# Kernel optimization log

Hardware: AMD Instinct MI355X
Metric: run time of the kernel (lower is better)

Reference implementation:

```python
import jax, jax.numpy as jnp
import numpy as np

NUM_USERS = 100000
NUM_MOVIES = 20000
FEAT = 256
H = 64
E = 2000000
EL = 500000


def _seg_mean(msg, dst, n):
    # scatter-mean aggregation: sum per destination node / neighbor count (clamped to 1)
    s = jax.ops.segment_sum(msg, dst, num_segments=n)
    c = jax.ops.segment_sum(jnp.ones((dst.shape[0], 1), msg.dtype), dst, num_segments=n)
    return s / jnp.maximum(c, 1.0)


def _sage(x_src, x_dst, src, dst, wl, bl, wr):
    # PyG SAGEConv (mean aggr): lin_l(mean_j x_j) + lin_r(x_i)
    mean = _seg_mean(x_src[src], dst, x_dst.shape[0])  # [N_dst, H]
    return mean @ wl + bl + x_dst @ wr


def _l2norm(x):
    n = jnp.linalg.norm(x, axis=-1, keepdims=True)
    return x / jnp.maximum(n, 1e-12)


def setup_inputs() -> dict:
    key = jax.random.key(0)
    ks = jax.random.split(key, 24)
    s = 0.02
    d = {
        'movie_x': jax.random.normal(ks[0], (NUM_MOVIES, FEAT), jnp.float32),
        'user_emb': jax.random.normal(ks[1], (NUM_USERS, H), jnp.float32) * s,
        'proj_w': jax.random.normal(ks[2], (FEAT, H), jnp.float32) * s,
        'proj_b': jnp.zeros((H,), jnp.float32),
        'c1_um_wl': jax.random.normal(ks[3], (H, H), jnp.float32) * s,
        'c1_um_bl': jnp.zeros((H,), jnp.float32),
        'c1_um_wr': jax.random.normal(ks[4], (H, H), jnp.float32) * s,
        'c1_mu_wl': jax.random.normal(ks[5], (H, H), jnp.float32) * s,
        'c1_mu_bl': jnp.zeros((H,), jnp.float32),
        'c1_mu_wr': jax.random.normal(ks[6], (H, H), jnp.float32) * s,
        'c2_um_wl': jax.random.normal(ks[7], (H, H), jnp.float32) * s,
        'c2_um_bl': jnp.zeros((H,), jnp.float32),
        'c2_um_wr': jax.random.normal(ks[8], (H, H), jnp.float32) * s,
        'c2_mu_wl': jax.random.normal(ks[9], (H, H), jnp.float32) * s,
        'c2_mu_bl': jnp.zeros((H,), jnp.float32),
        'c2_mu_wr': jax.random.normal(ks[10], (H, H), jnp.float32) * s,
        'dec_w1': jax.random.normal(ks[11], (2 * H, H), jnp.float32) * s,
        'dec_b1': jnp.zeros((H,), jnp.float32),
        'dec_w2': jax.random.normal(ks[12], (H, 1), jnp.float32) * s,
        'dec_b2': jnp.zeros((1,), jnp.float32),
        'edge_src': jax.random.randint(ks[13], (E,), 0, NUM_USERS, jnp.int32),
        'edge_dst': jax.random.randint(ks[14], (E,), 0, NUM_MOVIES, jnp.int32),
        'lbl_src': jax.random.randint(ks[15], (EL,), 0, NUM_USERS, jnp.int32),
        'lbl_dst': jax.random.randint(ks[16], (EL,), 0, NUM_MOVIES, jnp.int32),
    }
    return d


def reference(movie_x, user_emb, proj_w, proj_b,
              c1_um_wl, c1_um_bl, c1_um_wr, c1_mu_wl, c1_mu_bl, c1_mu_wr,
              c2_um_wl, c2_um_bl, c2_um_wr, c2_mu_wl, c2_mu_bl, c2_mu_wr,
              dec_w1, dec_b1, dec_w2, dec_b2,
              edge_src, edge_dst, lbl_src, lbl_dst):
    # node embeddings (dropout = identity, eval mode)
    user0 = user_emb                                   # [U, H]
    movie0 = jax.nn.relu(movie_x @ proj_w + proj_b)    # [M, H]
    # layer 1 hetero SAGE + relu + residual
    m1 = jax.nn.relu(_sage(user0, movie0, edge_src, edge_dst, c1_um_wl, c1_um_bl, c1_um_wr))
    u1 = jax.nn.relu(_sage(movie0, user0, edge_dst, edge_src, c1_mu_wl, c1_mu_bl, c1_mu_wr))
    u_res = user0 + u1
    m_res = movie0 + m1
    # layer 2 hetero SAGE
    m2 = _sage(u_res, m_res, edge_src, edge_dst, c2_um_wl, c2_um_bl, c2_um_wr)
    u2 = _sage(m_res, u_res, edge_dst, edge_src, c2_mu_wl, c2_mu_bl, c2_mu_wr)
    # L2-normalize, edge-gather decoder MLP
    u = _l2norm(u2)
    m = _l2norm(m2)
    x = jnp.concatenate([u[lbl_src], m[lbl_dst]], axis=-1)  # [EL, 2H]
    h = jax.nn.relu(x @ dec_w1 + dec_b1)
    return h @ dec_w2 + dec_b2                              # [EL, 1]
```

## Files before the change

kernel.cpp:

```cpp
#include <hip/hip_runtime.h>

#define NB 256
#define ND 256

typedef _Float16 f16x8 __attribute__((ext_vector_type(8)));
typedef _Float16 f16x4 __attribute__((ext_vector_type(4)));
typedef float f32x4 __attribute__((ext_vector_type(4)));

__device__ inline void wfrag128(const float* wl, const float* wr, f16x8* out, int idx) {
    int lane_i = idx & 63, t = idx >> 6;
    int col = (t & 3) * 16 + (lane_i & 15);
    int krow = (t >> 2) * 32 + ((lane_i >> 4) << 3);
    f16x8 v;
    #pragma unroll
    for (int j = 0; j < 8; ++j) {
        int k = krow + j;
        const float* W = (k < 64) ? (wl + (size_t)k * 64) : (wr + (size_t)(k - 64) * 64);
        v[j] = (_Float16)W[col];
    }
    out[t * 64 + lane_i] = v;
}
__device__ inline void wfrag64(const float* wd, f16x8* out, int idx) {
    int lane_i = idx & 63, t = idx >> 6;
    int col = (t & 3) * 16 + (lane_i & 15);
    int krow = (t >> 2) * 32 + ((lane_i >> 4) << 3);
    f16x8 v;
    #pragma unroll
    for (int j = 0; j < 8; ++j)
        v[j] = (_Float16)wd[(size_t)(krow + j) * 64 + col];
    out[t * 64 + lane_i] = v;
}

__global__ __launch_bounds__(1024) void k_init(const int* __restrict__ src, const int* __restrict__ dst,
                                               int* __restrict__ hist_u, int* __restrict__ hist_m,
                                               int E, int chunk,
                                               const float* __restrict__ c1mwl, const float* __restrict__ c1mwr,
                                               const float* __restrict__ c1uwl, const float* __restrict__ c1uwr,
                                               const float* __restrict__ c2mwl, const float* __restrict__ c2mwr,
                                               const float* __restrict__ c2uwl, const float* __restrict__ c2uwr,
                                               const float* __restrict__ decw1, const float* __restrict__ projw,
                                               const float* __restrict__ uemb,
                                               f16x8* __restrict__ wtab, _Float16* __restrict__ user16, int un4) {
    int b = blockIdx.x, tid = threadIdx.x;
    if (b < NB) {
        __shared__ int hu[ND], hm[ND];
        for (int t = tid; t < ND; t += 1024) { hu[t] = 0; hm[t] = 0; }
        __syncthreads();
        int e0 = b * chunk, e1 = min(E, e0 + chunk);
        for (int e = e0 + tid; e < e1; e += 1024) {
            atomicAdd(&hu[src[e] >> 9], 1);
            atomicAdd(&hm[dst[e] >> 7], 1);
        }
        __syncthreads();
        for (int t = tid; t < ND; t += 1024) {
            hist_u[t * NB + b] = hu[t];
            hist_m[t * NB + b] = hm[t];
        }
        return;
    }
    int p = (b - NB) * 1024 + tid;
    if (p < 4096) {
        int which = p >> 10, idx = p & 1023;
        const float* wl; const float* wr; f16x8* out;
        if (which == 0)      { wl = c1mwl; wr = c1mwr; out = wtab; }
        else if (which == 1) { wl = c1uwl; wr = c1uwr; out = wtab + 1024; }
        else if (which == 2) { wl = c2mwl; wr = c2mwr; out = wtab + 2048; }
        else                 { wl = c2uwl; wr = c2uwr; out = wtab + 3072; }
        wfrag128(wl, wr, out, idx);
    } else if (p < 5120) {
        int q = p - 4096;
        int which = q >> 9, idx = q & 511;
        wfrag64(which == 0 ? (decw1 + 64 * 64) : decw1, which == 0 ? wtab + 4096 : wtab + 4608, idx);
    } else if (p < 7168) {
        int idx = p - 5120;
        int lane_i = idx & 63, t = idx >> 6;
        int col = (t & 3) * 16 + (lane_i & 15);
        int krow = (t >> 2) * 32 + ((lane_i >> 4) << 3);
        f16x8 v;
        #pragma unroll
        for (int j = 0; j < 8; ++j)
            v[j] = (_Float16)projw[(size_t)(krow + j) * 64 + col];
        (wtab + 5120)[t * 64 + lane_i] = v;
    } else {
        int i = p - 7168;
        if (i < un4) {
            float4 v = ((const float4*)uemb)[i];
            ((f16x4*)user16)[i] = f16x4{(_Float16)v.x, (_Float16)v.y, (_Float16)v.z, (_Float16)v.w};
        }
    }
}

__global__ void k_scan_local2(const int* __restrict__ hist, int* __restrict__ scanned,
                              int* __restrict__ bsums, int NF) {
    __shared__ int s[1024];
    int side = blockIdx.x >> 6, b = blockIdx.x & 63;
    const int* in = hist + side * NF;
    int* outp = scanned + side * NF;
    int base = b * 1024;
    for (int t = threadIdx.x; t < 1024; t += 256) s[t] = in[base + t];
    __syncthreads();
    for (int d = 1; d < 1024; d <<= 1) {
        int vals[4];
        for (int j = 0; j < 4; ++j) {
            int t = threadIdx.x + j * 256;
            vals[j] = (t >= d) ? s[t - d] : 0;
        }
        __syncthreads();
        for (int j = 0; j < 4; ++j) {
            int t = threadIdx.x + j * 256;
            s[t] += vals[j];
        }
        __syncthreads();
    }
    for (int t = threadIdx.x; t < 1024; t += 256) outp[base + t] = s[t];
    if (threadIdx.x == 0) bsums[side * 64 + b] = s[1023];
}

__global__ void k_scan_carry2(int* bsums) {
    __shared__ int s[64];
    int* bs = bsums + blockIdx.x * 64;
    int t = threadIdx.x;
    if (t < 64) s[t] = bs[t];
    __syncthreads();
    if (t < 64) {
        int v = s[t];
        #pragma unroll
        for (int o = 1; o < 64; o <<= 1) {
            int u = __shfl_up(v, o, 64);
            if (t >= o) v += u;
        }
        bs[t] = v;
    }
}

__global__ void k_scan_off2(const int* __restrict__ scanned, const int* __restrict__ bsums,
                            int* __restrict__ off_m, int* __restrict__ off_u, int NF) {
    int idx = blockIdx.x * 256 + threadIdx.x;
    int side = idx / (NF + 1), i = idx - side * (NF + 1);
    if (side > 1) return;
    const int* sc = scanned + side * NF;
    const int* bs = bsums + side * 64;
    int v = 0;
    if (i > 0) {
        int j = i - 1, b = j >> 10;
        v = sc[j] + (b > 0 ? bs[b - 1] : 0);
    }
    (side ? off_u : off_m)[i] = v;
}

__global__ __launch_bounds__(1024) void k_scatter2(const int* __restrict__ src, const int* __restrict__ dst,
                                                   const int* __restrict__ off_flat_m, const int* __restrict__ off_flat_u,
                                                   int2* __restrict__ tmp_m, int2* __restrict__ tmp_u,
                                                   int E, int chunk) {
    __shared__ int cnt[ND];
    int side = blockIdx.x >= NB;
    int b = blockIdx.x & (NB - 1);
    const int* key = side ? src : dst;
    const int* val = side ? dst : src;
    const int* off = side ? off_flat_u : off_flat_m;
    int2* tmp = side ? tmp_u : tmp_m;
    int shift = side ? 9 : 7;
    for (int t = threadIdx.x; t < ND; t += 1024) cnt[t] = 0;
    __syncthreads();
    int e0 = b * chunk, e1 = min(E, e0 + chunk);
    for (int e = e0 + threadIdx.x; e < e1; e += 1024) {
        int k = key[e];
        int d = k >> shift;
        int r = atomicAdd(&cnt[d], 1);
        tmp[off[d * NB + b] + r] = make_int2(k, val[e]);
    }
}

__global__ __launch_bounds__(1024) void k_bucket2(const int2* __restrict__ tmp_m, const int2* __restrict__ tmp_u,
                                                  const int* __restrict__ off_flat_m, const int* __restrict__ off_flat_u,
                                                  int* __restrict__ adj_m, int* __restrict__ adj_u,
                                                  int* __restrict__ offn_m, int* __restrict__ offn_u,
                                                  int E, int M, int U) {
    __shared__ int cnt[512];
    int side = blockIdx.x >= ND;
    int d = blockIdx.x & (ND - 1);
    const int2* tmp = side ? tmp_u : tmp_m;
    const int* off_flat = side ? off_flat_u : off_flat_m;
    int* adj = side ? adj_u : adj_m;
    int* off_node = side ? offn_u : offn_m;
    int NN = side ? U : M;
    int shift = side ? 9 : 7;
    int width = 1 << shift;
    int bstart = off_flat[d * NB];
    int bend   = off_flat[(d + 1 == ND) ? (ND * NB) : ((d + 1) * NB)];
    for (int t = threadIdx.x; t < width; t += 1024) cnt[t] = 0;
    __syncthreads();
    int bsz = bend - bstart;
    for (int i = threadIdx.x; i < bsz; i += 1024)
        atomicAdd(&cnt[tmp[bstart + i].x & (width - 1)], 1);
    __syncthreads();
    int lane = threadIdx.x;
    if (lane < 64) {
        int EPL = width >> 6;
        int vals[8];
        int tot = 0;
        #pragma unroll
        for (int j = 0; j < 8; ++j) {
            vals[j] = (j < EPL) ? cnt[lane * EPL + j] : 0;
            tot += vals[j];
        }
        int inc = tot;
        #pragma unroll
        for (int o = 1; o < 64; o <<= 1) {
            int tsh = __shfl_up(inc, o, 64);
            if (lane >= o) inc += tsh;
        }
        int ex = inc - tot;
        #pragma unroll
        for (int j = 0; j < 8; ++j) {
            if (j < EPL) { cnt[lane * EPL + j] = ex; ex += vals[j]; }
        }
    }
    __syncthreads();
    int base_node = d << shift;
    for (int t = threadIdx.x; t < width; t += 1024) {
        int node = base_node + t;
        if (node < NN) off_node[node] = bstart + cnt[t];
    }
    if (d == 0 && threadIdx.x == 0) off_node[NN] = E;
    __syncthreads();
    for (int i = threadIdx.x; i < bsz; i += 1024) {
        int2 e = tmp[bstart + i];
        int r = atomicAdd(&cnt[e.x & (width - 1)], 1);
        adj[bstart + r] = e.y;
    }
}

__global__ __launch_bounds__(256, 4) void k_proj_mfma(const float* __restrict__ mx,
                                                      const f16x8* __restrict__ wfrag,
                                                      const float* __restrict__ b,
                                                      _Float16* __restrict__ out16, int M) {
    __shared__ f16x8 wf[32 * 64];
    const int tid = threadIdx.x;
    for (int t = tid; t < 2048; t += 256)
        ((float4*)wf)[t] = ((const float4*)wfrag)[t];
    __syncthreads();
    const int w = tid >> 6, lane = tid & 63;
    const int g = lane >> 4, c15 = lane & 15;
    const int w16 = w * 16;
    float blv[4];
    #pragma unroll
    for (int nt = 0; nt < 4; ++nt) blv[nt] = b[nt * 16 + c15];
    f16x8 afz;
    #pragma unroll
    for (int j = 0; j < 8; ++j) afz[j] = (_Float16)0.f;
    for (int n0 = blockIdx.x * 64; n0 < M; n0 += gridDim.x * 64) {
        int na = n0 + w16 + c15;
        f32x4 acc[4];
        #pragma unroll
        for (int nt = 0; nt < 4; ++nt) acc[nt] = f32x4{0.f, 0.f, 0.f, 0.f};
        #pragma unroll
        for (int kt = 0; kt < 8; ++kt) {
            f16x8 af = afz;
            if (na < M) {
                const float* row = mx + (size_t)na * 256 + kt * 32 + g * 8;
                float4 a = *(const float4*)row, bq = *(const float4*)(row + 4);
                af = f16x8{(_Float16)a.x, (_Float16)a.y, (_Float16)a.z, (_Float16)a.w,
                           (_Float16)bq.x, (_Float16)bq.y, (_Float16)bq.z, (_Float16)bq.w};
            }
            #pragma unroll
            for (int nt = 0; nt < 4; ++nt)
                acc[nt] = __builtin_amdgcn_mfma_f32_16x16x32_f16(af, wf[(kt * 4 + nt) * 64 + lane],
                                                                 acc[nt], 0, 0, 0);
        }
        #pragma unroll
        for (int nt = 0; nt < 4; ++nt) {
            #pragma unroll
            for (int r = 0; r < 4; ++r) {
                int n = n0 + w16 + g * 4 + r;
                if (n < M)
                    out16[(size_t)n * 64 + nt * 16 + c15] = (_Float16)fmaxf(acc[nt][r] + blv[nt], 0.f);
            }
        }
    }
}

__global__ __launch_bounds__(256) void k_agg2(const _Float16* __restrict__ xm,
                                              const int* __restrict__ adj_m, const int* __restrict__ off_m,
                                              _Float16* __restrict__ out_m, int M,
                                              const _Float16* __restrict__ xu,
                                              const int* __restrict__ adj_u, const int* __restrict__ off_u,
                                              _Float16* __restrict__ out_u, int U, int gm4) {
    int bid = blockIdx.x;
    int side = bid >= gm4;
    const _Float16* x = side ? xu : xm;
    const int* adj = side ? adj_u : adj_m;
    const int* off = side ? off_u : off_m;
    _Float16* out16 = side ? out_u : out_m;
    int N = side ? U : M;
    int node = (side ? bid - gm4 : bid) * 4 + (threadIdx.x >> 6);
    if (node >= N) return;
    int lane = threadIdx.x & 63;
    int g = lane >> 3;
    int i = lane & 7;
    int s0 = off[node], s1 = off[node + 1];
    f16x8 acc0, acc1;
    #pragma unroll
    for (int j = 0; j < 8; ++j) { acc0[j] = (_Float16)0.f; acc1[j] = (_Float16)0.f; }
    int e = s0 + g;
    for (; e + 8 < s1; e += 16) {
        f16x8 v = ((const f16x8*)x)[(size_t)adj[e] * 8 + i];
        f16x8 w = ((const f16x8*)x)[(size_t)adj[e + 8] * 8 + i];
        acc0 += v;
        acc1 += w;
    }
    if (e < s1) {
        f16x8 v = ((const f16x8*)x)[(size_t)adj[e] * 8 + i];
        acc0 += v;
    }
    float f[8];
    #pragma unroll
    for (int j = 0; j < 8; ++j) f[j] = (float)acc0[j] + (float)acc1[j];
    #pragma unroll
    for (int o = 8; o <= 32; o <<= 1) {
        #pragma unroll
        for (int j = 0; j < 8; ++j) f[j] += __shfl_xor(f[j], o, 64);
    }
    int deg = s1 - s0;
    float scale = (deg > 0) ? 1.0f / (float)deg : 0.f;
    if (g == 0) {
        f16x8 r;
        #pragma unroll
        for (int j = 0; j < 8; ++j) r[j] = (_Float16)(f[j] * scale);
        ((f16x8*)out16)[(size_t)node * 8 + i] = r;
    }
}

__global__ __launch_bounds__(256, 6) void k_trans1x(const _Float16* __restrict__ mean_m,
                                                    const _Float16* __restrict__ self_m,
                                                    const f16x8* __restrict__ wf_m,
                                                    const float* __restrict__ bl_m,
                                                    _Float16* __restrict__ res_m, int M,
                                                    const _Float16* __restrict__ mean_u,
                                                    const _Float16* __restrict__ self_u,
                                                    const f16x8* __restrict__ wf_u,
                                                    const float* __restrict__ bl_u,
                                                    _Float16* __restrict__ res_u, int U, int GM) {
    __shared__ f16x8 wf[16 * 64];
    int bid = blockIdx.x;
    int side = bid >= GM;
    const _Float16* mean16 = side ? mean_u : mean_m;
    const _Float16* self16 = side ? self_u : self_m;
    const f16x8* wfrag = side ? wf_u : wf_m;
    const float* bl = side ? bl_u : bl_m;
    _Float16* res16 = side ? res_u : res_m;
    int N = side ? U : M;
    int n0 = (side ? bid - GM : bid) * 64;
    const int tid = threadIdx.x;
    for (int t = tid; t < 1024; t += 256)
        ((float4*)wf)[t] = ((const float4*)wfrag)[t];
    __syncthreads();
    const int w = tid >> 6, lane = tid & 63;
    const int g = lane >> 4, c15 = lane & 15;
    const int w16 = w * 16;
    float blv[4];
    #pragma unroll
    for (int nt = 0; nt < 4; ++nt) blv[nt] = bl[nt * 16 + c15];
    f16x8 afz;
    #pragma unroll
    for (int j = 0; j < 8; ++j) afz[j] = (_Float16)0.f;
    int na = n0 + w16 + c15;
    f16x8 af[4] = {afz, afz, afz, afz};
    if (na < N) {
        const _Float16* mrow = mean16 + (size_t)na * 64 + g * 8;
        const _Float16* srow = self16 + (size_t)na * 64 + g * 8;
        af[0] = *(const f16x8*)mrow;
        af[1] = *(const f16x8*)(mrow + 32);
        af[2] = *(const f16x8*)srow;
        af[3] = *(const f16x8*)(srow + 32);
    }
    f32x4 acc[4];
    #pragma unroll
    for (int nt = 0; nt < 4; ++nt) acc[nt] = f32x4{0.f, 0.f, 0.f, 0.f};
    #pragma unroll
    for (int kt = 0; kt < 4; ++kt) {
        #pragma unroll
        for (int nt = 0; nt < 4; ++nt)
            acc[nt] = __builtin_amdgcn_mfma_f32_16x16x32_f16(af[kt], wf[(kt * 4 + nt) * 64 + lane],
                                                             acc[nt], 0, 0, 0);
    }
    #pragma unroll
    for (int nt = 0; nt < 4; ++nt) {
        #pragma unroll
        for (int r = 0; r < 4; ++r) {
            int n = n0 + w16 + g * 4 + r;
            if (n < N) {
                size_t o = (size_t)n * 64 + nt * 16 + c15;
                res16[o] = (_Float16)((float)self16[o] + fmaxf(acc[nt][r] + blv[nt], 0.f));
            }
        }
    }
}

__global__ __launch_bounds__(256, 4) void k_trans2x(const _Float16* __restrict__ mean_m,
                                                    const _Float16* __restrict__ res_m,
                                                    const f16x8* __restrict__ wf_m,
                                                    const f16x8* __restrict__ wd_m,
                                                    const float* __restrict__ bl_m,
                                                    _Float16* __restrict__ out_m, int M,
                                                    const _Float16* __restrict__ mean_u,
                                                    const _Float16* __restrict__ res_u,
                                                    const f16x8* __restrict__ wf_u,
                                                    const f16x8* __restrict__ wd_u,
                                                    const float* __restrict__ bl_u,
                                                    _Float16* __restrict__ out_u, int U, int GM) {
    __shared__ f16x8 wf[16 * 64];
    __shared__ f16x8 wf2[8 * 64];
    __shared__ _Float16 xs2[64][72];
    int bid = blockIdx.x;
    int side = bid >= GM;
    const _Float16* mean16 = side ? mean_u : mean_m;
    const _Float16* res16 = side ? res_u : res_m;
    const f16x8* wfrag = side ? wf_u : wf_m;
    const f16x8* wdfrag = side ? wd_u : wd_m;
    const float* bl = side ? bl_u : bl_m;
    _Float16* outA16 = side ? out_u : out_m;
    int N = side ? U : M;
    int n0 = (side ? bid - GM : bid) * 64;
    const int tid = threadIdx.x;
    for (int t = tid; t < 1024; t += 256)
        ((float4*)wf)[t] = ((const float4*)wfrag)[t];
    for (int t = tid; t < 512; t += 256)
        ((float4*)wf2)[t] = ((const float4*)wdfrag)[t];
    __syncthreads();
    const int w = tid >> 6, lane = tid & 63;
    const int g = lane >> 4, c15 = lane & 15;
    const int w16 = w * 16;
    float blv[4];
    #pragma unroll
    for (int nt = 0; nt < 4; ++nt) blv[nt] = bl[nt * 16 + c15];
    f16x8 afz;
    #pragma unroll
    for (int j = 0; j < 8; ++j) afz[j] = (_Float16)0.f;
    int na = n0 + w16 + c15;
    f16x8 af[4] = {afz, afz, afz, afz};
    if (na < N) {
        const _Float16* mrow = mean16 + (size_t)na * 64 + g * 8;
        const _Float16* rrow = res16 + (size_t)na * 64 + g * 8;
        af[0] = *(const f16x8*)mrow;
        af[1] = *(const f16x8*)(mrow + 32);
        af[2] = *(const f16x8*)rrow;
        af[3] = *(const f16x8*)(rrow + 32);
    }
    f32x4 acc[4];
    #pragma unroll
    for (int nt = 0; nt < 4; ++nt) acc[nt] = f32x4{0.f, 0.f, 0.f, 0.f};
    #pragma unroll
    for (int kt = 0; kt < 4; ++kt) {
        #pragma unroll
        for (int nt = 0; nt < 4; ++nt)
            acc[nt] = __builtin_amdgcn_mfma_f32_16x16x32_f16(af[kt], wf[(kt * 4 + nt) * 64 + lane],
                                                             acc[nt], 0, 0, 0);
    }
    float u2[4][4];
    #pragma unroll
    for (int nt = 0; nt < 4; ++nt)
        #pragma unroll
        for (int r = 0; r < 4; ++r)
            u2[nt][r] = acc[nt][r] + blv[nt];
    float sc[4];
    #pragma unroll
    for (int r = 0; r < 4; ++r) {
        float q = u2[0][r] * u2[0][r] + u2[1][r] * u2[1][r]
                + u2[2][r] * u2[2][r] + u2[3][r] * u2[3][r];
        q += __shfl_xor(q, 1, 64);
        q += __shfl_xor(q, 2, 64);
        q += __shfl_xor(q, 4, 64);
        q += __shfl_xor(q, 8, 64);
        sc[r] = 1.f / fmaxf(sqrtf(q), 1e-12f);
    }
    #pragma unroll
    for (int nt = 0; nt < 4; ++nt)
        #pragma unroll
        for (int r = 0; r < 4; ++r)
            xs2[w16 + g * 4 + r][nt * 16 + c15] = (_Float16)(u2[nt][r] * sc[r]);
    f32x4 acc2[4];
    #pragma unroll
    for (int nt = 0; nt < 4; ++nt) acc2[nt] = f32x4{0.f, 0.f, 0.f, 0.f};
    #pragma unroll
    for (int kt = 0; kt < 2; ++kt) {
        f16x8 af2 = *(const f16x8*)&xs2[w16 + c15][kt * 32 + (g << 3)];
        #pragma unroll
        for (int nt = 0; nt < 4; ++nt)
            acc2[nt] = __builtin_amdgcn_mfma_f32_16x16x32_f16(af2, wf2[(kt * 4 + nt) * 64 + lane],
                                                              acc2[nt], 0, 0, 0);
    }
    #pragma unroll
    for (int nt = 0; nt < 4; ++nt) {
        #pragma unroll
        for (int r = 0; r < 4; ++r) {
            int n = n0 + w16 + g * 4 + r;
            if (n < N)
                outA16[(size_t)n * 64 + nt * 16 + c15] = (_Float16)acc2[nt][r];
        }
    }
}

__global__ __launch_bounds__(256) void k_dec_h(const _Float16* __restrict__ A,
                                               const _Float16* __restrict__ B,
                                               const int* __restrict__ ls,
                                               const int* __restrict__ ld,
                                               const float* __restrict__ b1,
                                               const float* __restrict__ w2,
                                               const float* __restrict__ b2,
                                               float* __restrict__ out, int EL) {
    int lane = threadIdx.x & 63;
    int g = lane >> 3, i = lane & 7;
    int e = blockIdx.x * 32 + (threadIdx.x >> 6) * 8 + g;
    if (e >= EL) return;
    int u = ls[e], m = ld[e];
    f16x8 av = ((const f16x8*)A)[(size_t)u * 8 + i];
    f16x8 bv = ((const f16x8*)B)[(size_t)m * 8 + i];
    float4 b1a = ((const float4*)b1)[i * 2], b1b = ((const float4*)b1)[i * 2 + 1];
    float4 w2a = ((const float4*)w2)[i * 2], w2b = ((const float4*)w2)[i * 2 + 1];
    float p = 0.f;
    #pragma unroll
    for (int j = 0; j < 4; ++j) {
        p += fmaxf((float)av[j] + (float)bv[j] + (&b1a.x)[j], 0.f) * (&w2a.x)[j];
        p += fmaxf((float)av[j + 4] + (float)bv[j + 4] + (&b1b.x)[j], 0.f) * (&w2b.x)[j];
    }
    p += __shfl_xor(p, 1, 64);
    p += __shfl_xor(p, 2, 64);
    p += __shfl_xor(p, 4, 64);
    if (i == 0) out[e] = p + b2[0];
}

extern "C" void kernel_launch(void* const* d_in, const int* in_sizes, int n_in,
                              void* d_out, int out_size, void* d_ws, size_t ws_size,
                              hipStream_t stream) {
    const float* movie_x  = (const float*)d_in[0];
    const float* user_emb = (const float*)d_in[1];
    const float* proj_w   = (const float*)d_in[2];
    const float* proj_b   = (const float*)d_in[3];
    const float* c1_um_wl = (const float*)d_in[4];
    const float* c1_um_bl = (const float*)d_in[5];
    const float* c1_um_wr = (const float*)d_in[6];
    const float* c1_mu_wl = (const float*)d_in[7];
    const float* c1_mu_bl = (const float*)d_in[8];
    const float* c1_mu_wr = (const float*)d_in[9];
    const float* c2_um_wl = (const float*)d_in[10];
    const float* c2_um_bl = (const float*)d_in[11];
    const float* c2_um_wr = (const float*)d_in[12];
    const float* c2_mu_wl = (const float*)d_in[13];
    const float* c2_mu_bl = (const float*)d_in[14];
    const float* c2_mu_wr = (const float*)d_in[15];
    const float* dec_w1   = (const float*)d_in[16];
    const float* dec_b1   = (const float*)d_in[17];
    const float* dec_w2   = (const float*)d_in[18];
    const float* dec_b2   = (const float*)d_in[19];
    const int* edge_src = (const int*)d_in[20];
    const int* edge_dst = (const int*)d_in[21];
    const int* lbl_src  = (const int*)d_in[22];
    const int* lbl_dst  = (const int*)d_in[23];

    const int M  = in_sizes[0] / 256;
    const int U  = in_sizes[1] / 64;
    const int E  = in_sizes[20];
    const int EL = in_sizes[22];
    float* out = (float*)d_out;

    char* ws = (char*)d_ws;
    size_t off = 0;
    auto alloc = [&](size_t bytes) -> void* {
        off = (off + 255) & ~(size_t)255;
        void* p = ws + off;
        off += bytes;
        return p;
    };
    const int NF = ND * NB;
    int* hist       = (int*)alloc((size_t)2 * NF * 4);
    int* scanned    = (int*)alloc((size_t)2 * NF * 4);
    int* bsums      = (int*)alloc(512);
    int* off_flat_m = (int*)alloc((size_t)(NF + 1) * 4);
    int* off_flat_u = (int*)alloc((size_t)(NF + 1) * 4);
    int2* tmp_m     = (int2*)alloc((size_t)E * 8);
    int2* tmp_u     = (int2*)alloc((size_t)E * 8);
    int* off_u  = (int*)alloc((size_t)(U + 1) * 4);
    int* off_m  = (int*)alloc((size_t)(M + 1) * 4);
    int* adj_u  = (int*)alloc((size_t)E * 4);
    int* adj_m  = (int*)alloc((size_t)E * 4);
    f16x8* wtab = (f16x8*)alloc(7168 * 16);
    _Float16* movie16  = (_Float16*)alloc((size_t)M * 64 * 2);
    _Float16* user16   = (_Float16*)alloc((size_t)U * 64 * 2);
    _Float16* mean16_m = (_Float16*)alloc((size_t)M * 64 * 2);
    _Float16* mean16_u = (_Float16*)alloc((size_t)U * 64 * 2);
    _Float16* m_res16  = (_Float16*)alloc((size_t)M * 64 * 2);
    _Float16* u_res16  = (_Float16*)alloc((size_t)U * 64 * 2);
    _Float16* A16 = (_Float16*)alloc((size_t)U * 64 * 2);
    _Float16* B16 = (_Float16*)alloc((size_t)M * 64 * 2);

    f16x8* wf1m = wtab;
    f16x8* wf1u = wtab + 1024;
    f16x8* wf2m = wtab + 2048;
    f16x8* wf2u = wtab + 3072;
    f16x8* wdm  = wtab + 4096;
    f16x8* wdu  = wtab + 4608;
    f16x8* wpj  = wtab + 5120;

    int* hist_m = hist;
    int* hist_u = hist + NF;

    auto cdiv = [](int a, int b) { return (a + b - 1) / b; };
    const int chunk = cdiv(E, NB);

    hipMemsetAsync(hist, 0, (size_t)2 * NF * 4, stream);
    k_init<<<NB + cdiv(7168 + U * 16, 1024), 1024, 0, stream>>>(
        edge_src, edge_dst, hist_u, hist_m, E, chunk,
        c1_um_wl, c1_um_wr, c1_mu_wl, c1_mu_wr,
        c2_um_wl, c2_um_wr, c2_mu_wl, c2_mu_wr,
        dec_w1, proj_w, user_emb, wtab, user16, U * 16);

    k_scan_local2<<<128, 256, 0, stream>>>(hist, scanned, bsums, NF);
    k_scan_carry2<<<2, 64, 0, stream>>>(bsums);
    k_scan_off2<<<cdiv(2 * (NF + 1), 256), 256, 0, stream>>>(scanned, bsums, off_flat_m, off_flat_u, NF);
    k_scatter2<<<2 * NB, 1024, 0, stream>>>(edge_src, edge_dst, off_flat_m, off_flat_u, tmp_m, tmp_u, E, chunk);
    k_bucket2<<<2 * ND, 1024, 0, stream>>>(tmp_m, tmp_u, off_flat_m, off_flat_u,
                                           adj_m, adj_u, off_m, off_u, E, M, U);

    int gm = cdiv(M, 64), gu = cdiv(U, 64);
    int gm4 = cdiv(M, 4), gu4 = cdiv(U, 4);

    k_proj_mfma<<<min(gm, 2048), 256, 0, stream>>>(movie_x, wpj, proj_b, movie16, M);

    k_agg2<<<gm4 + gu4, 256, 0, stream>>>(user16, adj_m, off_m, mean16_m, M,
                                          movie16, adj_u, off_u, mean16_u, U, gm4);
    k_trans1x<<<gm + gu, 256, 0, stream>>>(mean16_m, movie16, wf1m, c1_um_bl, m_res16, M,
                                           mean16_u, user16, wf1u, c1_mu_bl, u_res16, U, gm);

    k_agg2<<<gm4 + gu4, 256, 0, stream>>>(u_res16, adj_m, off_m, mean16_m, M,
                                          m_res16, adj_u, off_u, mean16_u, U, gm4);
    k_trans2x<<<gm + gu, 256, 0, stream>>>(mean16_m, m_res16, wf2m, wdm, c2_um_bl, B16, M,
                                           mean16_u, u_res16, wf2u, wdu, c2_mu_bl, A16, U, gm);

    k_dec_h<<<cdiv(EL, 32), 256, 0, stream>>>(A16, B16, lbl_src, lbl_dst,
                                              dec_b1, dec_w2, dec_b2, out, EL);
}
```

Baseline: 275.1 us.

## Pack bucket entries into 32-bit words and fuse movie projection into bucket kernel

```diff
diff --git a/kernel.cpp b/kernel.cpp
--- a/kernel.cpp
+++ b/kernel.cpp
@@ -150,7 +150,7 @@
 
 __global__ __launch_bounds__(1024) void k_scatter2(const int* __restrict__ src, const int* __restrict__ dst,
                                                    const int* __restrict__ off_flat_m, const int* __restrict__ off_flat_u,
-                                                   int2* __restrict__ tmp_m, int2* __restrict__ tmp_u,
+                                                   int* __restrict__ tmp_m, int* __restrict__ tmp_u,
                                                    int E, int chunk) {
     __shared__ int cnt[ND];
     int side = blockIdx.x >= NB;
@@ -158,8 +158,9 @@
     const int* key = side ? src : dst;
     const int* val = side ? dst : src;
     const int* off = side ? off_flat_u : off_flat_m;
-    int2* tmp = side ? tmp_u : tmp_m;
+    int* tmp = side ? tmp_u : tmp_m;
     int shift = side ? 9 : 7;
+    int wmask = (1 << shift) - 1;
     for (int t = threadIdx.x; t < ND; t += 1024) cnt[t] = 0;
     __syncthreads();
     int e0 = b * chunk, e1 = min(E, e0 + chunk);
@@ -167,115 +168,116 @@
         int k = key[e];
         int d = k >> shift;
         int r = atomicAdd(&cnt[d], 1);
-        tmp[off[d * NB + b] + r] = make_int2(k, val[e]);
-    }
-}
-
-__global__ __launch_bounds__(1024) void k_bucket2(const int2* __restrict__ tmp_m, const int2* __restrict__ tmp_u,
-                                                  const int* __restrict__ off_flat_m, const int* __restrict__ off_flat_u,
-                                                  int* __restrict__ adj_m, int* __restrict__ adj_u,
-                                                  int* __restrict__ offn_m, int* __restrict__ offn_u,
-                                                  int E, int M, int U) {
+        tmp[off[d * NB + b] + r] = ((k & wmask) << 17) | val[e];
+    }
+}
+
+__global__ __launch_bounds__(1024) void k_bucket_proj(const int* __restrict__ tmp_m, const int* __restrict__ tmp_u,
+                                                      const int* __restrict__ off_flat_m, const int* __restrict__ off_flat_u,
+                                                      int* __restrict__ adj_m, int* __restrict__ adj_u,
+                                                      int* __restrict__ offn_m, int* __restrict__ offn_u,
+                                                      int E, int M, int U,
+                                                      const float* __restrict__ mx,
+                                                      const f16x8* __restrict__ wpj,
+                                                      const float* __restrict__ pb,
+                                                      _Float16* __restrict__ movie16) {
     __shared__ int cnt[512];
-    int side = blockIdx.x >= ND;
-    int d = blockIdx.x & (ND - 1);
-    const int2* tmp = side ? tmp_u : tmp_m;
-    const int* off_flat = side ? off_flat_u : off_flat_m;
-    int* adj = side ? adj_u : adj_m;
-    int* off_node = side ? offn_u : offn_m;
-    int NN = side ? U : M;
-    int shift = side ? 9 : 7;
-    int width = 1 << shift;
-    int bstart = off_flat[d * NB];
-    int bend   = off_flat[(d + 1 == ND) ? (ND * NB) : ((d + 1) * NB)];
-    for (int t = threadIdx.x; t < width; t += 1024) cnt[t] = 0;
-    __syncthreads();
-    int bsz = bend - bstart;
-    for (int i = threadIdx.x; i < bsz; i += 1024)
-        atomicAdd(&cnt[tmp[bstart + i].x & (width - 1)], 1);
-    __syncthreads();
-    int lane = threadIdx.x;
-    if (lane < 64) {
-        int EPL = width >> 6;
-        int vals[8];
-        int tot = 0;
-        #pragma unroll
-        for (int j = 0; j < 8; ++j) {
-            vals[j] = (j < EPL) ? cnt[lane * EPL + j] : 0;
-            tot += vals[j];
-        }
-        int inc = tot;
-        #pragma unroll
-        for (int o = 1; o < 64; o <<= 1) {
-            int tsh = __shfl_up(inc, o, 64);
-            if (lane >= o) inc += tsh;
-        }
-        int ex = inc - tot;
-        #pragma unroll
-        for (int j = 0; j < 8; ++j) {
-            if (j < EPL) { cnt[lane * EPL + j] = ex; ex += vals[j]; }
-        }
-    }
-    __syncthreads();
-    int base_node = d << shift;
-    for (int t = threadIdx.x; t < width; t += 1024) {
-        int node = base_node + t;
-        if (node < NN) off_node[node] = bstart + cnt[t];
-    }
-    if (d == 0 && threadIdx.x == 0) off_node[NN] = E;
-    __syncthreads();
-    for (int i = threadIdx.x; i < bsz; i += 1024) {
-        int2 e = tmp[bstart + i];
-        int r = atomicAdd(&cnt[e.x & (width - 1)], 1);
-        adj[bstart + r] = e.y;
-    }
-}
-
-__global__ __launch_bounds__(256, 4) void k_proj_mfma(const float* __restrict__ mx,
-                                                      const f16x8* __restrict__ wfrag,
-                                                      const float* __restrict__ b,
-                                                      _Float16* __restrict__ out16, int M) {
-    __shared__ f16x8 wf[32 * 64];
-    const int tid = threadIdx.x;
-    for (int t = tid; t < 2048; t += 256)
-        ((float4*)wf)[t] = ((const float4*)wfrag)[t];
+    __shared__ f16x8 wf[2048];
+    int bid = blockIdx.x, tid = threadIdx.x;
+    if (bid < 2 * ND) {
+        int side = bid >= ND;
+        int d = bid & (ND - 1);
+        const int* tmp = side ? tmp_u : tmp_m;
+        const int* off_flat = side ? off_flat_u : off_flat_m;
+        int* adj = side ? adj_u : adj_m;
+        int* off_node = side ? offn_u : offn_m;
+        int NN = side ? U : M;
+        int shift = side ? 9 : 7;
+        int width = 1 << shift;
+        int bstart = off_flat[d * NB];
+        int bend   = off_flat[(d + 1 == ND) ? (ND * NB) : ((d + 1) * NB)];
+        for (int t = tid; t < width; t += 1024) cnt[t] = 0;
+        __syncthreads();
+        int bsz = bend - bstart;
+        for (int i = tid; i < bsz; i += 1024)
+            atomicAdd(&cnt[tmp[bstart + i] >> 17], 1);
+        __syncthreads();
+        int lane = tid;
+        if (lane < 64) {
+            int EPL = width >> 6;
+            int vals[8];
+            int tot = 0;
+            #pragma unroll
+            for (int j = 0; j < 8; ++j) {
+                vals[j] = (j < EPL) ? cnt[lane * EPL + j] : 0;
+                tot += vals[j];
+            }
+            int inc = tot;
+            #pragma unroll
+            for (int o = 1; o < 64; o <<= 1) {
+                int tsh = __shfl_up(inc, o, 64);
+                if (lane >= o) inc += tsh;
+            }
+            int ex = inc - tot;
+            #pragma unroll
+            for (int j = 0; j < 8; ++j) {
+                if (j < EPL) { cnt[lane * EPL + j] = ex; ex += vals[j]; }
+            }
+        }
+        __syncthreads();
+        int base_node = d << shift;
+        for (int t = tid; t < width; t += 1024) {
+            int node = base_node + t;
+            if (node < NN) off_node[node] = bstart + cnt[t];
+        }
+        if (d == 0 && tid == 0) off_node[NN] = E;
+        __syncthreads();
+        for (int i = tid; i < bsz; i += 1024) {
+            int v = tmp[bstart + i];
+            int r = atomicAdd(&cnt[v >> 17], 1);
+            adj[bstart + r] = v & 0x1FFFF;
+        }
+        return;
+    }
+    int pt = bid - 2 * ND;
+    for (int t = tid; t < 2048; t += 1024)
+        ((float4*)wf)[t] = ((const float4*)wpj)[t];
     __syncthreads();
     const int w = tid >> 6, lane = tid & 63;
     const int g = lane >> 4, c15 = lane & 15;
     const int w16 = w * 16;
+    int n0 = pt * 256;
     float blv[4];
     #pragma unroll
-    for (int nt = 0; nt < 4; ++nt) blv[nt] = b[nt * 16 + c15];
+    for (int nt = 0; nt < 4; ++nt) blv[nt] = pb[nt * 16 + c15];
     f16x8 afz;
     #pragma unroll
     for (int j = 0; j < 8; ++j) afz[j] = (_Float16)0.f;
-    for (int n0 = blockIdx.x * 64; n0 < M; n0 += gridDim.x * 64) {
-        int na = n0 + w16 + c15;
-        f32x4 acc[4];
-        #pragma unroll
-        for (int nt = 0; nt < 4; ++nt) acc[nt] = f32x4{0.f, 0.f, 0.f, 0.f};
-        #pragma unroll
-        for (int kt = 0; kt < 8; ++kt) {
-            f16x8 af = afz;
-            if (na < M) {
-                const float* row = mx + (size_t)na * 256 + kt * 32 + g * 8;
-                float4 a = *(const float4*)row, bq = *(const float4*)(row + 4);
-                af = f16x8{(_Float16)a.x, (_Float16)a.y, (_Float16)a.z, (_Float16)a.w,
-                           (_Float16)bq.x, (_Float16)bq.y, (_Float16)bq.z, (_Float16)bq.w};
-            }
-            #pragma unroll
-            for (int nt = 0; nt < 4; ++nt)
-                acc[nt] = __builtin_amdgcn_mfma_f32_16x16x32_f16(af, wf[(kt * 4 + nt) * 64 + lane],
-                                                                 acc[nt], 0, 0, 0);
-        }
-        #pragma unroll
-        for (int nt = 0; nt < 4; ++nt) {
-            #pragma unroll
-            for (int r = 0; r < 4; ++r) {
-                int n = n0 + w16 + g * 4 + r;
-                if (n < M)
-                    out16[(size_t)n * 64 + nt * 16 + c15] = (_Float16)fmaxf(acc[nt][r] + blv[nt], 0.f);
-            }
+    int na = n0 + w16 + c15;
+    f32x4 acc[4];
+    #pragma unroll
+    for (int nt = 0; nt < 4; ++nt) acc[nt] = f32x4{0.f, 0.f, 0.f, 0.f};
+    #pragma unroll
+    for (int kt = 0; kt < 8; ++kt) {
+        f16x8 af = afz;
+        if (na < M) {
+            const float* row = mx + (size_t)na * 256 + kt * 32 + g * 8;
+            float4 a = *(const float4*)row, bq = *(const float4*)(row + 4);
+            af = f16x8{(_Float16)a.x, (_Float16)a.y, (_Float16)a.z, (_Float16)a.w,
+                       (_Float16)bq.x, (_Float16)bq.y, (_Float16)bq.z, (_Float16)bq.w};
+        }
+        #pragma unroll
+        for (int nt = 0; nt < 4; ++nt)
+            acc[nt] = __builtin_amdgcn_mfma_f32_16x16x32_f16(af, wf[(kt * 4 + nt) * 64 + lane],
+                                                             acc[nt], 0, 0, 0);
+    }
+    #pragma unroll
+    for (int nt = 0; nt < 4; ++nt) {
+        #pragma unroll
+        for (int r = 0; r < 4; ++r) {
+            int n = n0 + w16 + g * 4 + r;
+            if (n < M)
+                movie16[(size_t)n * 64 + nt * 16 + c15] = (_Float16)fmaxf(acc[nt][r] + blv[nt], 0.f);
         }
     }
 }
@@ -578,8 +580,8 @@
     int* bsums      = (int*)alloc(512);
     int* off_flat_m = (int*)alloc((size_t)(NF + 1) * 4);
     int* off_flat_u = (int*)alloc((size_t)(NF + 1) * 4);
-    int2* tmp_m     = (int2*)alloc((size_t)E * 8);
-    int2* tmp_u     = (int2*)alloc((size_t)E * 8);
+    int* tmp_m      = (int*)alloc((size_t)E * 4);
+    int* tmp_u      = (int*)alloc((size_t)E * 4);
     int* off_u  = (int*)alloc((size_t)(U + 1) * 4);
     int* off_m  = (int*)alloc((size_t)(M + 1) * 4);
     int* adj_u  = (int*)alloc((size_t)E * 4);
@@ -619,13 +621,14 @@
     k_scan_carry2<<<2, 64, 0, stream>>>(bsums);
     k_scan_off2<<<cdiv(2 * (NF + 1), 256), 256, 0, stream>>>(scanned, bsums, off_flat_m, off_flat_u, NF);
     k_scatter2<<<2 * NB, 1024, 0, stream>>>(edge_src, edge_dst, off_flat_m, off_flat_u, tmp_m, tmp_u, E, chunk);
-    k_bucket2<<<2 * ND, 1024, 0, stream>>>(tmp_m, tmp_u, off_flat_m, off_flat_u,
-                                           adj_m, adj_u, off_m, off_u, E, M, U);
 
     int gm = cdiv(M, 64), gu = cdiv(U, 64);
     int gm4 = cdiv(M, 4), gu4 = cdiv(U, 4);
 
-    k_proj_mfma<<<min(gm, 2048), 256, 0, stream>>>(movie_x, wpj, proj_b, movie16, M);
+    k_bucket_proj<<<2 * ND + cdiv(M, 256), 1024, 0, stream>>>(
+        tmp_m, tmp_u, off_flat_m, off_flat_u,
+        adj_m, adj_u, off_m, off_u, E, M, U,
+        movie_x, wpj, proj_b, movie16);
 
     k_agg2<<<gm4 + gu4, 256, 0, stream>>>(user16, adj_m, off_m, mean16_m, M,
                                           movie16, adj_u, off_u, mean16_u, U, gm4);
```

Result: faster. 257.7 us (-6.3%).
